# Optimization experiments

Hardware: AMD Instinct MI355X
Metric: run time of the kernel (lower is better)

The kernel has to match this reference:

```python
import jax, jax.numpy as jnp
import numpy as np

B, S, D, H, DFF = 2, 2048, 2048, 16, 8192
DH = D // H
EPS = 1e-5


def _layer_norm(x, g, b):
    mu = jnp.mean(x, axis=-1, keepdims=True)
    var = jnp.mean(jnp.square(x - mu), axis=-1, keepdims=True)
    return (x - mu) * jax.lax.rsqrt(var + EPS) * g + b


def setup_inputs() -> dict:
    key = jax.random.key(0)
    ks = jax.random.split(key, 12)
    sc = 0.02
    inp = {
        "x": jax.random.normal(ks[0], (B, S, D), dtype=jnp.float32),
        # attention projections, stored [in, out] (torch Linear weight transposed)
        "wq": jax.random.normal(ks[1], (D, D), dtype=jnp.float32) * sc,
        "bq": jnp.zeros((D,), jnp.float32),
        "wk": jax.random.normal(ks[2], (D, D), dtype=jnp.float32) * sc,
        "bk": jnp.zeros((D,), jnp.float32),
        "wv": jax.random.normal(ks[3], (D, D), dtype=jnp.float32) * sc,
        "bv": jnp.zeros((D,), jnp.float32),
        "wo": jax.random.normal(ks[4], (D, D), dtype=jnp.float32) * sc,
        "bo": jnp.zeros((D,), jnp.float32),
        "ln1_g": jnp.ones((D,), jnp.float32),
        "ln1_b": jnp.zeros((D,), jnp.float32),
        # feed-forward
        "w1": jax.random.normal(ks[5], (D, DFF), dtype=jnp.float32) * sc,
        "b1": jnp.zeros((DFF,), jnp.float32),
        "w2": jax.random.normal(ks[6], (DFF, D), dtype=jnp.float32) * sc,
        "b2": jnp.zeros((D,), jnp.float32),
        "ln2_g": jnp.ones((D,), jnp.float32),
        "ln2_b": jnp.zeros((D,), jnp.float32),
    }
    return inp


def reference(x, wq, bq, wk, bk, wv, bv, wo, bo, ln1_g, ln1_b,
              w1, b1, w2, b2, ln2_g, ln2_b):
    # ---- MultiHeadAttentionBlock: x + MHA(LN(x)) ----
    h = _layer_norm(x, ln1_g, ln1_b)                      # [B,S,D]
    q = (h @ wq + bq).reshape(B, S, H, DH).transpose(0, 2, 1, 3)  # [B,H,S,DH]
    k = (h @ wk + bk).reshape(B, S, H, DH).transpose(0, 2, 1, 3)
    v = (h @ wv + bv).reshape(B, S, H, DH).transpose(0, 2, 1, 3)

    # faithful to source: scale by sqrt(d_dim), NOT sqrt(head_dim)
    scores = jnp.einsum("bhqd,bhkd->bhqk", q, k) / np.sqrt(D).astype(np.float32)
    # faithful triu/transpose masking (softmax sees raw zeros, not -inf)
    t = jnp.triu(scores).swapaxes(-2, -1)                 # [B,H,S,S]
    s = jax.nn.softmax(t, axis=-2)
    r = jnp.triu(s).swapaxes(-2, -1)
    attn = jnp.einsum("bhqk,bhkd->bhqd", r, v)            # [B,H,S,DH]
    attn = attn.transpose(0, 2, 1, 3).reshape(B, S, D)
    x = x + attn @ wo + bo

    # ---- FeedForwardBlock: x + FF(LN(x)), dropout rate 0 ----
    h2 = _layer_norm(x, ln2_g, ln2_b)
    ff = jax.nn.relu(h2 @ w1 + b1) @ w2 + b2
    return x + ff
```

## Files before the change

### kernel.cpp

```cpp
#include <hip/hip_runtime.h>


typedef unsigned short ushort_t;
typedef unsigned int   uint32;
typedef __attribute__((ext_vector_type(8)))  short    short8;
typedef __attribute__((ext_vector_type(8)))  ushort_t ushort8;
typedef __attribute__((ext_vector_type(4)))  float    f32x4;

#define BDIM   2
#define SEQ    2048
#define DMODEL 2048
#define NHEAD  16
#define DHEAD  128
#define DFFN   8192
#define MROWS  (BDIM*SEQ)
#define LDQKV  6144

#define GPTR(p) (const __attribute__((address_space(1))) void*)((const void*)(p))
#define SPTR(p) (__attribute__((address_space(3))) void*)((void*)(p))

__device__ __forceinline__ float bf2f(ushort_t u) {
  union { uint32 i; float f; } c; c.i = ((uint32)u) << 16; return c.f;
}
__device__ __forceinline__ ushort_t f2bf(float f) {
  union { float f; uint32 i; } c; c.f = f;
  uint32 u = c.i;
  return (ushort_t)((u + 0x7fffu + ((u >> 16) & 1u)) >> 16);
}

__global__ __launch_bounds__(256) void prep_kern(
    const float* __restrict__ wq, const float* __restrict__ wk,
    const float* __restrict__ wv, const float* __restrict__ wo,
    const float* __restrict__ w1, const float* __restrict__ w2,
    const float* __restrict__ bq, const float* __restrict__ bk,
    const float* __restrict__ bv,
    ushort_t* __restrict__ WQKV, ushort_t* __restrict__ WOT,
    ushort_t* __restrict__ W1T, ushort_t* __restrict__ W2T,
    float* __restrict__ Bcat)
{
  const int bid = blockIdx.x;
  if (bid >= 49152) {
    for (int i = threadIdx.x; i < 6144; i += 256)
      Bcat[i] = (i < 2048) ? bq[i] : ((i < 4096) ? bk[i - 2048] : bv[i - 4096]);
    return;
  }
  const float* W; ushort_t* Wt; int K, N, local;
  if (bid < 12288) {
    const int which = bid >> 12; local = bid & 4095;
    W = (which == 0) ? wq : (which == 1) ? wk : wv;
    Wt = WQKV + (size_t)which * 2048 * 2048; K = 2048; N = 2048;
  } else if (bid < 16384) { W = wo; Wt = WOT; K = 2048; N = 2048; local = bid - 12288; }
  else if (bid < 32768)   { W = w1; Wt = W1T; K = 2048; N = 8192; local = bid - 16384; }
  else                    { W = w2; Wt = W2T; K = 8192; N = 2048; local = bid - 32768; }
  const int ntiles = N >> 5;
  const int nb = (local % ntiles) * 32, kb = (local / ntiles) * 32;

  __shared__ float tile[32][33];
  const int tx = threadIdx.x & 31, ty = threadIdx.x >> 5;
#pragma unroll
  for (int j = 0; j < 32; j += 8)
    tile[ty + j][tx] = W[(size_t)(kb + ty + j) * N + nb + tx];
  __syncthreads();
#pragma unroll
  for (int j = 0; j < 32; j += 8)
    Wt[(size_t)(nb + ty + j) * K + kb + tx] = f2bf(tile[tx][ty + j]);
}

__global__ __launch_bounds__(256) void ln_kern(
    const float* __restrict__ X, const float* __restrict__ G,
    const float* __restrict__ Bb, ushort_t* __restrict__ Out)
{
  const int row = blockIdx.x, tid = threadIdx.x;
  const float* xr = X + (size_t)row * DMODEL;
  float4 v0 = ((const float4*)xr)[tid * 2];
  float4 v1 = ((const float4*)xr)[tid * 2 + 1];
  float s  = v0.x + v0.y + v0.z + v0.w + v1.x + v1.y + v1.z + v1.w;
  float ss = v0.x*v0.x + v0.y*v0.y + v0.z*v0.z + v0.w*v0.w
           + v1.x*v1.x + v1.y*v1.y + v1.z*v1.z + v1.w*v1.w;
#pragma unroll
  for (int off = 32; off > 0; off >>= 1) {
    s  += __shfl_down(s, off);
    ss += __shfl_down(ss, off);
  }
  __shared__ float rs[4], rss[4];
  __shared__ float sh_mu, sh_rst;
  const int wv = tid >> 6;
  if ((tid & 63) == 0) { rs[wv] = s; rss[wv] = ss; }
  __syncthreads();
  if (tid == 0) {
    float S1 = rs[0] + rs[1] + rs[2] + rs[3];
    float S2 = rss[0] + rss[1] + rss[2] + rss[3];
    float mu = S1 * (1.f / DMODEL);
    float var = S2 * (1.f / DMODEL) - mu * mu;
    sh_mu = mu;
    sh_rst = rsqrtf(var + 1e-5f);
  }
  __syncthreads();
  const float mu = sh_mu, rst = sh_rst;
  float4 g0 = ((const float4*)G)[tid * 2];
  float4 g1 = ((const float4*)G)[tid * 2 + 1];
  float4 b0 = ((const float4*)Bb)[tid * 2];
  float4 b1 = ((const float4*)Bb)[tid * 2 + 1];
  ushort8 o;
  o[0] = f2bf((v0.x - mu) * rst * g0.x + b0.x);
  o[1] = f2bf((v0.y - mu) * rst * g0.y + b0.y);
  o[2] = f2bf((v0.z - mu) * rst * g0.z + b0.z);
  o[3] = f2bf((v0.w - mu) * rst * g0.w + b0.w);
  o[4] = f2bf((v1.x - mu) * rst * g1.x + b1.x);
  o[5] = f2bf((v1.y - mu) * rst * g1.y + b1.y);
  o[6] = f2bf((v1.z - mu) * rst * g1.z + b1.z);
  o[7] = f2bf((v1.w - mu) * rst * g1.w + b1.w);
  *(ushort8*)(Out + (size_t)row * DMODEL + tid * 8) = o;
}

__global__ __launch_bounds__(256) void combine_ln_kern(
    const ushort_t* __restrict__ pp, const float* __restrict__ bias,
    const float* __restrict__ xres, const float* __restrict__ G,
    const float* __restrict__ Bb, float* __restrict__ X2,
    ushort_t* __restrict__ Out)
{
  const int row = blockIdx.x, tid = threadIdx.x;
  const size_t i = (size_t)row * DMODEL + tid * 8;
  ushort8 p0 = *(const ushort8*)(pp + i);
  ushort8 p1 = *(const ushort8*)(pp + (size_t)MROWS * 2048 + i);
  float v[8];
#pragma unroll
  for (int j = 0; j < 8; ++j)
    v[j] = bf2f(p0[j]) + bf2f(p1[j]) + bias[tid * 8 + j] + xres[i + j];
  float4 o0 = {v[0], v[1], v[2], v[3]}, o1 = {v[4], v[5], v[6], v[7]};
  *(float4*)(X2 + i) = o0;
  *(float4*)(X2 + i + 4) = o1;

  float s = 0.f, ss = 0.f;
#pragma unroll
  for (int j = 0; j < 8; ++j) { s += v[j]; ss += v[j] * v[j]; }
#pragma unroll
  for (int off = 32; off > 0; off >>= 1) {
    s  += __shfl_down(s, off);
    ss += __shfl_down(ss, off);
  }
  __shared__ float rs[4], rss[4];
  __shared__ float sh_mu, sh_rst;
  const int wvv = tid >> 6;
  if ((tid & 63) == 0) { rs[wvv] = s; rss[wvv] = ss; }
  __syncthreads();
  if (tid == 0) {
    float S1 = rs[0] + rs[1] + rs[2] + rs[3];
    float S2 = rss[0] + rss[1] + rss[2] + rss[3];
    float mu = S1 * (1.f / DMODEL);
    float var = S2 * (1.f / DMODEL) - mu * mu;
    sh_mu = mu; sh_rst = rsqrtf(var + 1e-5f);
  }
  __syncthreads();
  const float mu = sh_mu, rst = sh_rst;
  ushort8 o;
#pragma unroll
  for (int j = 0; j < 8; ++j)
    o[j] = f2bf((v[j] - mu) * rst * G[tid * 8 + j] + Bb[tid * 8 + j]);
  *(ushort8*)(Out + i) = o;
}

template<int OUT, int RELU, int KDIV>
__global__ __launch_bounds__(512, 2) void gemm8_kern(
    const ushort_t* __restrict__ A, const ushort_t* __restrict__ Bt,
    const float* __restrict__ bias, void* __restrict__ Cout,
    int M, int N, int K)
{
  __shared__ ushort_t sA[4 * 8192];
  __shared__ ushort_t sB[4 * 8192];

  const int tid = threadIdx.x;
  const int nM  = gridDim.y;
  const int nwg = gridDim.x * nM;
  const int bid = blockIdx.y * gridDim.x + blockIdx.x;
  const int cpx = nwg >> 3;
  const int swz = (bid & 7) * cpx + (bid >> 3);
  const int m0 = (swz % nM) * 256;
  const int n0 = (swz / nM) * 256;

  const int Keff = K / KDIV;
  const int k0 = (KDIV > 1) ? blockIdx.z * Keff : 0;
  const int T = Keff >> 6;

  const int l = tid & 63, w = tid >> 6;
  const int lr = l & 15, lg = l >> 4;
  const int wr = w >> 2, wc = w & 3;

  const int xch   = (lg ^ ((lr >> 1) & 3)) * 8;
  const int abase = (wr * 128 + lr) * 32 + xch;
  const int bbase = (wc * 64  + lr) * 32 + xch;

  const int sr = tid >> 2;
  const int sg = ((tid & 3) ^ ((tid >> 3) & 3)) * 8;
  const ushort_t* Asrc = A  + (size_t)(m0 + sr) * K + k0 + sg;
  const ushort_t* Bsrc = Bt + (size_t)(n0 + sr) * K + k0 + sg;
  ushort_t* dA = sA + tid * 8;
  ushort_t* dB = sB + tid * 8;

#define SA_(slot, kt, kk, r) __builtin_amdgcn_global_load_lds( \
    GPTR(Asrc + (size_t)(r) * 128 * K + (kt) * 64 + (kk) * 32), \
    SPTR(dA + (slot) * 8192 + (r) * 4096), 16, 0, 0)
#define SB_(slot, kt, kk, r) __builtin_amdgcn_global_load_lds( \
    GPTR(Bsrc + (size_t)(r) * 128 * K + (kt) * 64 + (kk) * 32), \
    SPTR(dB + (slot) * 8192 + (r) * 4096), 16, 0, 0)

  f32x4 acc[8][4] = {};

  SA_(0, 0, 0, 0); SA_(0, 0, 0, 1); SB_(0, 0, 0, 0); SB_(0, 0, 0, 1);
  SA_(1, 0, 1, 0); SA_(1, 0, 1, 1); SB_(1, 0, 1, 0); SB_(1, 0, 1, 1);
  SA_(2, 1, 0, 0); SA_(2, 1, 0, 1); SB_(2, 1, 0, 0); SB_(2, 1, 0, 1);
  asm volatile("s_waitcnt vmcnt(8)" ::: "memory");
  __builtin_amdgcn_s_barrier();

  for (int t = 0; t < T; ++t) {
    const int c = t & 1;
    const ushort_t* A0 = sA + (c * 2 + 0) * 8192;
    const ushort_t* B0 = sB + (c * 2 + 0) * 8192;
    const ushort_t* A1 = sA + (c * 2 + 1) * 8192;
    const ushort_t* B1 = sB + (c * 2 + 1) * 8192;
    const int s1 = (c ^ 1) * 2 + 1;
    const int s0 = c * 2;
    const bool pf1 = (t + 1 < T), pf0 = (t + 2 < T);
    const bool last2 = (t >= T - 2);

    short8 a0, a1, a2, a3, b0, b1, b2, b3;

    b0 = *(const short8*)(B0 + bbase);
    b1 = *(const short8*)(B0 + bbase + 512);
    b2 = *(const short8*)(B0 + bbase + 1024);
    b3 = *(const short8*)(B0 + bbase + 1536);
    a0 = *(const short8*)(A0 + abase);
    a1 = *(const short8*)(A0 + abase + 512);
    a2 = *(const short8*)(A0 + abase + 1024);
    a3 = *(const short8*)(A0 + abase + 1536);
    if (pf1) { SA_(s1, t + 1, 1, 0); SA_(s1, t + 1, 1, 1); }
    __builtin_amdgcn_s_barrier();
    asm volatile("s_waitcnt lgkmcnt(0)" ::: "memory");
    __builtin_amdgcn_s_setprio(1);
    acc[0][0] = __builtin_amdgcn_mfma_f32_16x16x32_bf16(a0, b0, acc[0][0], 0, 0, 0);
    acc[0][1] = __builtin_amdgcn_mfma_f32_16x16x32_bf16(a0, b1, acc[0][1], 0, 0, 0);
    acc[0][2] = __builtin_amdgcn_mfma_f32_16x16x32_bf16(a0, b2, acc[0][2], 0, 0, 0);
    acc[0][3] = __builtin_amdgcn_mfma_f32_16x16x32_bf16(a0, b3, acc[0][3], 0, 0, 0);
    acc[1][0] = __builtin_amdgcn_mfma_f32_16x16x32_bf16(a1, b0, acc[1][0], 0, 0, 0);
    acc[1][1] = __builtin_amdgcn_mfma_f32_16x16x32_bf16(a1, b1, acc[1][1], 0, 0, 0);
    acc[1][2] = __builtin_amdgcn_mfma_f32_16x16x32_bf16(a1, b2, acc[1][2], 0, 0, 0);
    acc[1][3] = __builtin_amdgcn_mfma_f32_16x16x32_bf16(a1, b3, acc[1][3], 0, 0, 0);
    acc[2][0] = __builtin_amdgcn_mfma_f32_16x16x32_bf16(a2, b0, acc[2][0], 0, 0, 0);
    acc[2][1] = __builtin_amdgcn_mfma_f32_16x16x32_bf16(a2, b1, acc[2][1], 0, 0, 0);
    acc[2][2] = __builtin_amdgcn_mfma_f32_16x16x32_bf16(a2, b2, acc[2][2], 0, 0, 0);
    acc[2][3] = __builtin_amdgcn_mfma_f32_16x16x32_bf16(a2, b3, acc[2][3], 0, 0, 0);
    acc[3][0] = __builtin_amdgcn_mfma_f32_16x16x32_bf16(a3, b0, acc[3][0], 0, 0, 0);
    acc[3][1] = __builtin_amdgcn_mfma_f32_16x16x32_bf16(a3, b1, acc[3][1], 0, 0, 0);
    acc[3][2] = __builtin_amdgcn_mfma_f32_16x16x32_bf16(a3, b2, acc[3][2], 0, 0, 0);
    acc[3][3] = __builtin_amdgcn_mfma_f32_16x16x32_bf16(a3, b3, acc[3][3], 0, 0, 0);
    __builtin_amdgcn_s_setprio(0);
    __builtin_amdgcn_s_barrier();

    a0 = *(const short8*)(A0 + abase + 2048);
    a1 = *(const short8*)(A0 + abase + 2560);
    a2 = *(const short8*)(A0 + abase + 3072);
    a3 = *(const short8*)(A0 + abase + 3584);
    if (pf1) { SB_(s1, t + 1, 1, 0); SB_(s1, t + 1, 1, 1); }
    __builtin_amdgcn_s_barrier();
    asm volatile("s_waitcnt lgkmcnt(0)" ::: "memory");
    __builtin_amdgcn_s_setprio(1);
    acc[4][0] = __builtin_amdgcn_mfma_f32_16x16x32_bf16(a0, b0, acc[4][0], 0, 0, 0);
    acc[4][1] = __builtin_amdgcn_mfma_f32_16x16x32_bf16(a0, b1, acc[4][1], 0, 0, 0);
    acc[4][2] = __builtin_amdgcn_mfma_f32_16x16x32_bf16(a0, b2, acc[4][2], 0, 0, 0);
    acc[4][3] = __builtin_amdgcn_mfma_f32_16x16x32_bf16(a0, b3, acc[4][3], 0, 0, 0);
    acc[5][0] = __builtin_amdgcn_mfma_f32_16x16x32_bf16(a1, b0, acc[5][0], 0, 0, 0);
    acc[5][1] = __builtin_amdgcn_mfma_f32_16x16x32_bf16(a1, b1, acc[5][1], 0, 0, 0);
    acc[5][2] = __builtin_amdgcn_mfma_f32_16x16x32_bf16(a1, b2, acc[5][2], 0, 0, 0);
    acc[5][3] = __builtin_amdgcn_mfma_f32_16x16x32_bf16(a1, b3, acc[5][3], 0, 0, 0);
    acc[6][0] = __builtin_amdgcn_mfma_f32_16x16x32_bf16(a2, b0, acc[6][0], 0, 0, 0);
    acc[6][1] = __builtin_amdgcn_mfma_f32_16x16x32_bf16(a2, b1, acc[6][1], 0, 0, 0);
    acc[6][2] = __builtin_amdgcn_mfma_f32_16x16x32_bf16(a2, b2, acc[6][2], 0, 0, 0);
    acc[6][3] = __builtin_amdgcn_mfma_f32_16x16x32_bf16(a2, b3, acc[6][3], 0, 0, 0);
    acc[7][0] = __builtin_amdgcn_mfma_f32_16x16x32_bf16(a3, b0, acc[7][0], 0, 0, 0);
    acc[7][1] = __builtin_amdgcn_mfma_f32_16x16x32_bf16(a3, b1, acc[7][1], 0, 0, 0);
    acc[7][2] = __builtin_amdgcn_mfma_f32_16x16x32_bf16(a3, b2, acc[7][2], 0, 0, 0);
    acc[7][3] = __builtin_amdgcn_mfma_f32_16x16x32_bf16(a3, b3, acc[7][3], 0, 0, 0);
    __builtin_amdgcn_s_setprio(0);
    if (!last2) { asm volatile("s_waitcnt vmcnt(8)" ::: "memory"); }
    else        { asm volatile("s_waitcnt vmcnt(0)" ::: "memory"); }
    __builtin_amdgcn_s_barrier();

    b0 = *(const short8*)(B1 + bbase);
    b1 = *(const short8*)(B1 + bbase + 512);
    b2 = *(const short8*)(B1 + bbase + 1024);
    b3 = *(const short8*)(B1 + bbase + 1536);
    a0 = *(const short8*)(A1 + abase);
    a1 = *(const short8*)(A1 + abase + 512);
    a2 = *(const short8*)(A1 + abase + 1024);
    a3 = *(const short8*)(A1 + abase + 1536);
    if (pf0) { SA_(s0, t + 2, 0, 0); SA_(s0, t + 2, 0, 1); }
    __builtin_amdgcn_s_barrier();
    asm volatile("s_waitcnt lgkmcnt(0)" ::: "memory");
    __builtin_amdgcn_s_setprio(1);
    acc[0][0] = __builtin_amdgcn_mfma_f32_16x16x32_bf16(a0, b0, acc[0][0], 0, 0, 0);
    acc[0][1] = __builtin_amdgcn_mfma_f32_16x16x32_bf16(a0, b1, acc[0][1], 0, 0, 0);
    acc[0][2] = __builtin_amdgcn_mfma_f32_16x16x32_bf16(a0, b2, acc[0][2], 0, 0, 0);
    acc[0][3] = __builtin_amdgcn_mfma_f32_16x16x32_bf16(a0, b3, acc[0][3], 0, 0, 0);
    acc[1][0] = __builtin_amdgcn_mfma_f32_16x16x32_bf16(a1, b0, acc[1][0], 0, 0, 0);
    acc[1][1] = __builtin_amdgcn_mfma_f32_16x16x32_bf16(a1, b1, acc[1][1], 0, 0, 0);
    acc[1][2] = __builtin_amdgcn_mfma_f32_16x16x32_bf16(a1, b2, acc[1][2], 0, 0, 0);
    acc[1][3] = __builtin_amdgcn_mfma_f32_16x16x32_bf16(a1, b3, acc[1][3], 0, 0, 0);
    acc[2][0] = __builtin_amdgcn_mfma_f32_16x16x32_bf16(a2, b0, acc[2][0], 0, 0, 0);
    acc[2][1] = __builtin_amdgcn_mfma_f32_16x16x32_bf16(a2, b1, acc[2][1], 0, 0, 0);
    acc[2][2] = __builtin_amdgcn_mfma_f32_16x16x32_bf16(a2, b2, acc[2][2], 0, 0, 0);
    acc[2][3] = __builtin_amdgcn_mfma_f32_16x16x32_bf16(a2, b3, acc[2][3], 0, 0, 0);
    acc[3][0] = __builtin_amdgcn_mfma_f32_16x16x32_bf16(a3, b0, acc[3][0], 0, 0, 0);
    acc[3][1] = __builtin_amdgcn_mfma_f32_16x16x32_bf16(a3, b1, acc[3][1], 0, 0, 0);
    acc[3][2] = __builtin_amdgcn_mfma_f32_16x16x32_bf16(a3, b2, acc[3][2], 0, 0, 0);
    acc[3][3] = __builtin_amdgcn_mfma_f32_16x16x32_bf16(a3, b3, acc[3][3], 0, 0, 0);
    __builtin_amdgcn_s_setprio(0);
    __builtin_amdgcn_s_barrier();

    a0 = *(const short8*)(A1 + abase + 2048);
    a1 = *(const short8*)(A1 + abase + 2560);
    a2 = *(const short8*)(A1 + abase + 3072);
    a3 = *(const short8*)(A1 + abase + 3584);
    if (pf0) { SB_(s0, t + 2, 0, 0); SB_(s0, t + 2, 0, 1); }
    __builtin_amdgcn_s_barrier();
    asm volatile("s_waitcnt lgkmcnt(0)" ::: "memory");
    __builtin_amdgcn_s_setprio(1);
    acc[4][0] = __builtin_amdgcn_mfma_f32_16x16x32_bf16(a0, b0, acc[4][0], 0, 0, 0);
    acc[4][1] = __builtin_amdgcn_mfma_f32_16x16x32_bf16(a0, b1, acc[4][1], 0, 0, 0);
    acc[4][2] = __builtin_amdgcn_mfma_f32_16x16x32_bf16(a0, b2, acc[4][2], 0, 0, 0);
    acc[4][3] = __builtin_amdgcn_mfma_f32_16x16x32_bf16(a0, b3, acc[4][3], 0, 0, 0);
    acc[5][0] = __builtin_amdgcn_mfma_f32_16x16x32_bf16(a1, b0, acc[5][0], 0, 0, 0);
    acc[5][1] = __builtin_amdgcn_mfma_f32_16x16x32_bf16(a1, b1, acc[5][1], 0, 0, 0);
    acc[5][2] = __builtin_amdgcn_mfma_f32_16x16x32_bf16(a1, b2, acc[5][2], 0, 0, 0);
    acc[5][3] = __builtin_amdgcn_mfma_f32_16x16x32_bf16(a1, b3, acc[5][3], 0, 0, 0);
    acc[6][0] = __builtin_amdgcn_mfma_f32_16x16x32_bf16(a2, b0, acc[6][0], 0, 0, 0);
    acc[6][1] = __builtin_amdgcn_mfma_f32_16x16x32_bf16(a2, b1, acc[6][1], 0, 0, 0);
    acc[6][2] = __builtin_amdgcn_mfma_f32_16x16x32_bf16(a2, b2, acc[6][2], 0, 0, 0);
    acc[6][3] = __builtin_amdgcn_mfma_f32_16x16x32_bf16(a2, b3, acc[6][3], 0, 0, 0);
    acc[7][0] = __builtin_amdgcn_mfma_f32_16x16x32_bf16(a3, b0, acc[7][0], 0, 0, 0);
    acc[7][1] = __builtin_amdgcn_mfma_f32_16x16x32_bf16(a3, b1, acc[7][1], 0, 0, 0);
    acc[7][2] = __builtin_amdgcn_mfma_f32_16x16x32_bf16(a3, b2, acc[7][2], 0, 0, 0);
    acc[7][3] = __builtin_amdgcn_mfma_f32_16x16x32_bf16(a3, b3, acc[7][3], 0, 0, 0);
    __builtin_amdgcn_s_setprio(0);
    if (!last2) { asm volatile("s_waitcnt vmcnt(8)" ::: "memory"); }
    else        { asm volatile("s_waitcnt vmcnt(0)" ::: "memory"); }
    __builtin_amdgcn_s_barrier();
  }
#undef SA_
#undef SB_

  ushort_t* Pz = (OUT == 2)
      ? (ushort_t*)Cout + (size_t)blockIdx.z * M * N : (ushort_t*)Cout;
#pragma unroll
  for (int mi = 0; mi < 8; ++mi) {
#pragma unroll
    for (int ni = 0; ni < 4; ++ni) {
      const int gn = n0 + wc * 64 + ni * 16 + lr;
      const float bvv = (OUT == 2) ? 0.f : bias[gn];
#pragma unroll
      for (int j = 0; j < 4; ++j) {
        const int gm = m0 + wr * 128 + mi * 16 + lg * 4 + j;
        float v = acc[mi][ni][j] + bvv;
        if (RELU) v = fmaxf(v, 0.f);
        Pz[(size_t)gm * N + gn] = f2bf(v);
      }
    }
  }
}

__global__ __launch_bounds__(256) void combine_kern(
    const ushort_t* __restrict__ pp, const float* __restrict__ bias,
    const float* __restrict__ resid, float* __restrict__ out)
{
  const size_t i = ((size_t)blockIdx.x * 256 + threadIdx.x) * 8;
  ushort8 p0 = *(const ushort8*)(pp + i);
  ushort8 p1 = *(const ushort8*)(pp + (size_t)MROWS * 2048 + i);
  const int col = (int)(i & 2047);
  float4 r0 = *(const float4*)(resid + i);
  float4 r1 = *(const float4*)(resid + i + 4);
  float4 c0 = *(const float4*)(bias + col);
  float4 c1 = *(const float4*)(bias + col + 4);
  float4 o0, o1;
  o0.x = bf2f(p0[0]) + bf2f(p1[0]) + c0.x + r0.x;
  o0.y = bf2f(p0[1]) + bf2f(p1[1]) + c0.y + r0.y;
  o0.z = bf2f(p0[2]) + bf2f(p1[2]) + c0.z + r0.z;
  o0.w = bf2f(p0[3]) + bf2f(p1[3]) + c0.w + r0.w;
  o1.x = bf2f(p0[4]) + bf2f(p1[4]) + c1.x + r1.x;
  o1.y = bf2f(p0[5]) + bf2f(p1[5]) + c1.y + r1.y;
  o1.z = bf2f(p0[6]) + bf2f(p1[6]) + c1.z + r1.z;
  o1.w = bf2f(p0[7]) + bf2f(p1[7]) + c1.w + r1.w;
  *(float4*)(out + i) = o0;
  *(float4*)(out + i + 4) = o1;
}

__global__ __launch_bounds__(256) void attn_stats_kern(
    const ushort_t* __restrict__ Q, const ushort_t* __restrict__ Kb,
    float* __restrict__ E, float* __restrict__ DG, int ld)
{
  __shared__ ushort_t Ksm[64 * 128];
  const int qb = blockIdx.x;
  const int bh = blockIdx.y;
  const int b = bh >> 4, h = bh & 15;
  const int tid = threadIdx.x;
  const int l = tid & 63, w = tid >> 6;
  const int lr = l & 15, lg = l >> 4;

  const int qrow0 = qb * 128 + w * 32;

  short8 af[2][4];
#pragma unroll
  for (int g = 0; g < 2; ++g) {
    const size_t qoff = (size_t)(b * SEQ + qrow0 + g * 16 + lr) * ld + h * DHEAD + lg * 8;
#pragma unroll
    for (int c = 0; c < 4; ++c) af[g][c] = *(const short8*)(Q + qoff + c * 32);
  }

  const int srow_b = w * 16 + (l >> 4);
  const ushort_t* Kg = Kb + (size_t)b * SEQ * ld + (size_t)h * DHEAD;
  ushort_t* Sbase = Ksm + w * 2048;

  f32x4 sume[2] = {{0.f,0.f,0.f,0.f},{0.f,0.f,0.f,0.f}};
  f32x4 dge[2]  = {{0.f,0.f,0.f,0.f},{0.f,0.f,0.f,0.f}};
  const float scale = 0.0220970869120796f;
  const int rx = lr & 7;

  for (int kc = qb * 2; kc < 32; ++kc) {
    __syncthreads();
#pragma unroll
    for (int c = 0; c < 4; ++c) {
      const int row = srow_b + c * 4;
      const int g = (l & 15) ^ (row & 7);
      __builtin_amdgcn_global_load_lds(
          GPTR(Kg + (size_t)(kc * 64 + row) * ld + g * 8),
          SPTR(Sbase + c * 512), 16, 0, 0);
    }
    __syncthreads();

    for (int ks = 0; ks < 4; ++ks) {
      const int kbase = kc * 64 + ks * 16;
      if (kbase + 16 <= qrow0) continue;
      short8 bfr[4];
#pragma unroll
      for (int c = 0; c < 4; ++c)
        bfr[c] = *(const short8*)(Ksm + (ks * 16 + lr) * 128 + ((lg + c * 4) ^ rx) * 8);
#pragma unroll
      for (int g = 0; g < 2; ++g) {
        const int qg = qrow0 + g * 16;
        if (kbase < qg) continue;
        f32x4 sc = {0.f, 0.f, 0.f, 0.f};
        sc = __builtin_amdgcn_mfma_f32_16x16x32_bf16(af[g][0], bfr[0], sc, 0, 0, 0);
        sc = __builtin_amdgcn_mfma_f32_16x16x32_bf16(af[g][1], bfr[1], sc, 0, 0, 0);
        sc = __builtin_amdgcn_mfma_f32_16x16x32_bf16(af[g][2], bfr[2], sc, 0, 0, 0);
        sc = __builtin_amdgcn_mfma_f32_16x16x32_bf16(af[g][3], bfr[3], sc, 0, 0, 0);
        if (kbase == qg) {
          const int ki = kbase + lr;
#pragma unroll
          for (int j = 0; j < 4; ++j) {
            const int qi = qg + lg * 4 + j;
            if (ki >= qi) {
              float e = __expf(sc[j] * scale);
              sume[g][j] += e;
              if (ki == qi) dge[g][j] += e;
            }
          }
        } else {
#pragma unroll
          for (int j = 0; j < 4; ++j)
            sume[g][j] += __expf(sc[j] * scale);
        }
      }
    }
  }

#pragma unroll
  for (int g = 0; g < 2; ++g) {
#pragma unroll
    for (int j = 0; j < 4; ++j) {
#pragma unroll
      for (int off = 1; off < 16; off <<= 1) {
        sume[g][j] += __shfl_xor(sume[g][j], off);
        dge[g][j]  += __shfl_xor(dge[g][j], off);
      }
    }
  }
  if (lr == 0) {
#pragma unroll
    for (int g = 0; g < 2; ++g)
#pragma unroll
      for (int j = 0; j < 4; ++j) {
        E[(size_t)bh * SEQ + qrow0 + g * 16 + lg * 4 + j]  = sume[g][j];
        DG[(size_t)bh * SEQ + qrow0 + g * 16 + lg * 4 + j] = dge[g][j];
      }
  }
}

__global__ __launch_bounds__(128) void vchunk_kern(
    const ushort_t* __restrict__ V, float* __restrict__ CS, int ld)
{
  const int c = blockIdx.x, bh = blockIdx.y;
  const int b = bh >> 4, h = bh & 15;
  const int dh = threadIdx.x;
  const ushort_t* vp = V + (size_t)(b * SEQ + c * 64) * ld + h * DHEAD + dh;
  float s = 0.f;
  for (int i = 0; i < 64; ++i) s += bf2f(vp[(size_t)i * ld]);
  CS[((size_t)bh * 32 + c) * 128 + dh] = s;
}

__global__ __launch_bounds__(128) void attn_combine_kern(
    const ushort_t* __restrict__ V, const float* __restrict__ CS,
    const float* __restrict__ E, const float* __restrict__ DG,
    ushort_t* __restrict__ Attn, int ldv)
{
  const int c = blockIdx.x, bh = blockIdx.y;
  const int b = bh >> 4, h = bh & 15;
  const int dh = threadIdx.x;
  float prefix = 0.f;
  for (int cc = 0; cc < c; ++cc) prefix += CS[((size_t)bh * 32 + cc) * 128 + dh];
  const ushort_t* vp = V + (size_t)(b * SEQ + c * 64) * ldv + h * DHEAD + dh;
  ushort_t* ap = Attn + (size_t)(b * SEQ + c * 64) * DMODEL + h * DHEAD + dh;
  const int qb = c * 64;
  for (int i = 0; i < 64; ++i) {
    const int qq = qb + i;
    const float denom = (float)qq + E[(size_t)bh * SEQ + qq];
    const float de = DG[(size_t)bh * SEQ + qq];
    const float vv = bf2f(vp[(size_t)i * ldv]);
    ap[(size_t)i * DMODEL] = f2bf((prefix + de * vv) / denom);
    prefix += vv;
  }
}

extern "C" void kernel_launch(void* const* d_in, const int* in_sizes, int n_in,
                              void* d_out, int out_size, void* d_ws, size_t ws_size,
                              hipStream_t stream)
{
  const float* x    = (const float*)d_in[0];
  const float* wq   = (const float*)d_in[1];
  const float* bq   = (const float*)d_in[2];
  const float* wk   = (const float*)d_in[3];
  const float* bk   = (const float*)d_in[4];
  const float* wv   = (const float*)d_in[5];
  const float* bv   = (const float*)d_in[6];
  const float* wo   = (const float*)d_in[7];
  const float* bo   = (const float*)d_in[8];
  const float* ln1g = (const float*)d_in[9];
  const float* ln1b = (const float*)d_in[10];
  const float* w1   = (const float*)d_in[11];
  const float* b1   = (const float*)d_in[12];
  const float* w2   = (const float*)d_in[13];
  const float* b2   = (const float*)d_in[14];
  const float* ln2g = (const float*)d_in[15];
  const float* ln2b = (const float*)d_in[16];
  float* out = (float*)d_out;

  char* ws = (char*)d_ws;
  ushort_t* W1T  = (ushort_t*)(ws + 0);
  ushort_t* PPf2 = (ushort_t*)(ws + 0);
  ushort_t* W2T  = (ushort_t*)(ws + 33554432);
  ushort_t* WOT  = (ushort_t*)(ws + 67108864);
  float*    X2   = (float*)   (ws + 75497472);
  float*    Bcat = (float*)   (ws + 75497472);
  ushort_t* Hb   = (ushort_t*)(ws + 109051904);
  ushort_t* F1   = (ushort_t*)(ws + 125829120);
  ushort_t* PPwo = (ushort_t*)(ws + 125829120);
  ushort_t* WQKV = (ushort_t*)(ws + 125829120);
  ushort_t* QKVb = (ushort_t*)(ws + 150994944);
  float*    Eb   = (float*)   (ws + 201326592);
  float*    DGb  = (float*)   (ws + 201588736);
  float*    CSb  = (float*)   (ws + 201850880);

  prep_kern<<<49153, 256, 0, stream>>>(wq, wk, wv, wo, w1, w2, bq, bk, bv,
                                       WQKV, WOT, W1T, W2T, Bcat);

  ln_kern<<<MROWS, 256, 0, stream>>>(x, ln1g, ln1b, Hb);

  gemm8_kern<1, 0, 1><<<dim3(24, 16), 512, 0, stream>>>(
      Hb, WQKV, Bcat, QKVb, MROWS, LDQKV, DMODEL);

  attn_stats_kern<<<dim3(16, 32), 256, 0, stream>>>(QKVb, QKVb + 2048, Eb, DGb, LDQKV);

  vchunk_kern<<<dim3(32, 32), 128, 0, stream>>>(QKVb + 4096, CSb, LDQKV);
  attn_combine_kern<<<dim3(32, 32), 128, 0, stream>>>(QKVb + 4096, CSb, Eb, DGb, Hb, LDQKV);

  gemm8_kern<2, 0, 2><<<dim3(8, 16, 2), 512, 0, stream>>>(
      Hb, WOT, bo, PPwo, MROWS, DMODEL, DMODEL);

  combine_ln_kern<<<MROWS, 256, 0, stream>>>(PPwo, bo, x, ln2g, ln2b, X2, Hb);

  gemm8_kern<1, 1, 1><<<dim3(32, 16), 512, 0, stream>>>(
      Hb, W1T, b1, F1, MROWS, DFFN, DMODEL);

  gemm8_kern<2, 0, 2><<<dim3(8, 16, 2), 512, 0, stream>>>(
      F1, W2T, b2, PPf2, MROWS, DMODEL, DFFN);
  combine_kern<<<4096, 256, 0, stream>>>(PPf2, b2, X2, out);
}
```

Before: 661.0 us.

## Drop intra-stage barriers in gemm8 and add triple-buffered 128x256 GEMM for FFN1

Removes the extra s_barrier and lgkmcnt waits around each MFMA half-step in the main GEMM kernel. Waves can then overlap their LDS reads and prefetch issue instead of lock-stepping. Adds a new GEMM kernel used only for the FFN up-projection, with a 128x256 tile, a 3-slot LDS ring buffer, a single barrier per K-step, and twice as many workgroups. The barrier removal relies on the remaining barriers still guarding slot reuse, so a hidden LDS race is a risk.

```diff
diff --git a/kernel.cpp b/kernel.cpp
--- a/kernel.cpp
+++ b/kernel.cpp
@@ -234,8 +234,6 @@
     a2 = *(const short8*)(A0 + abase + 1024);
     a3 = *(const short8*)(A0 + abase + 1536);
     if (pf1) { SA_(s1, t + 1, 1, 0); SA_(s1, t + 1, 1, 1); }
-    __builtin_amdgcn_s_barrier();
-    asm volatile("s_waitcnt lgkmcnt(0)" ::: "memory");
     __builtin_amdgcn_s_setprio(1);
     acc[0][0] = __builtin_amdgcn_mfma_f32_16x16x32_bf16(a0, b0, acc[0][0], 0, 0, 0);
     acc[0][1] = __builtin_amdgcn_mfma_f32_16x16x32_bf16(a0, b1, acc[0][1], 0, 0, 0);
@@ -254,15 +252,12 @@
     acc[3][2] = __builtin_amdgcn_mfma_f32_16x16x32_bf16(a3, b2, acc[3][2], 0, 0, 0);
     acc[3][3] = __builtin_amdgcn_mfma_f32_16x16x32_bf16(a3, b3, acc[3][3], 0, 0, 0);
     __builtin_amdgcn_s_setprio(0);
-    __builtin_amdgcn_s_barrier();
 
     a0 = *(const short8*)(A0 + abase + 2048);
     a1 = *(const short8*)(A0 + abase + 2560);
     a2 = *(const short8*)(A0 + abase + 3072);
     a3 = *(const short8*)(A0 + abase + 3584);
     if (pf1) { SB_(s1, t + 1, 1, 0); SB_(s1, t + 1, 1, 1); }
-    __builtin_amdgcn_s_barrier();
-    asm volatile("s_waitcnt lgkmcnt(0)" ::: "memory");
     __builtin_amdgcn_s_setprio(1);
     acc[4][0] = __builtin_amdgcn_mfma_f32_16x16x32_bf16(a0, b0, acc[4][0], 0, 0, 0);
     acc[4][1] = __builtin_amdgcn_mfma_f32_16x16x32_bf16(a0, b1, acc[4][1], 0, 0, 0);
@@ -294,8 +289,6 @@
     a2 = *(const short8*)(A1 + abase + 1024);
     a3 = *(const short8*)(A1 + abase + 1536);
     if (pf0) { SA_(s0, t + 2, 0, 0); SA_(s0, t + 2, 0, 1); }
-    __builtin_amdgcn_s_barrier();
-    asm volatile("s_waitcnt lgkmcnt(0)" ::: "memory");
     __builtin_amdgcn_s_setprio(1);
     acc[0][0] = __builtin_amdgcn_mfma_f32_16x16x32_bf16(a0, b0, acc[0][0], 0, 0, 0);
     acc[0][1] = __builtin_amdgcn_mfma_f32_16x16x32_bf16(a0, b1, acc[0][1], 0, 0, 0);
@@ -314,15 +307,12 @@
     acc[3][2] = __builtin_amdgcn_mfma_f32_16x16x32_bf16(a3, b2, acc[3][2], 0, 0, 0);
     acc[3][3] = __builtin_amdgcn_mfma_f32_16x16x32_bf16(a3, b3, acc[3][3], 0, 0, 0);
     __builtin_amdgcn_s_setprio(0);
-    __builtin_amdgcn_s_barrier();
 
     a0 = *(const short8*)(A1 + abase + 2048);
     a1 = *(const short8*)(A1 + abase + 2560);
     a2 = *(const short8*)(A1 + abase + 3072);
     a3 = *(const short8*)(A1 + abase + 3584);
     if (pf0) { SB_(s0, t + 2, 0, 0); SB_(s0, t + 2, 0, 1); }
-    __builtin_amdgcn_s_barrier();
-    asm volatile("s_waitcnt lgkmcnt(0)" ::: "memory");
     __builtin_amdgcn_s_setprio(1);
     acc[4][0] = __builtin_amdgcn_mfma_f32_16x16x32_bf16(a0, b0, acc[4][0], 0, 0, 0);
     acc[4][1] = __builtin_amdgcn_mfma_f32_16x16x32_bf16(a0, b1, acc[4][1], 0, 0, 0);
@@ -367,6 +357,98 @@
   }
 }
 
+template<int RELU>
+__global__ __launch_bounds__(512) void gemm_hi_kern(
+    const ushort_t* __restrict__ A, const ushort_t* __restrict__ Bt,
+    const float* __restrict__ bias, ushort_t* __restrict__ Cout,
+    int M, int N, int K)
+{
+  __shared__ ushort_t sA[3 * 4096];
+  __shared__ ushort_t sB[3 * 8192];
+
+  const int tid = threadIdx.x;
+  const int nM  = gridDim.y;
+  const int nwg = gridDim.x * nM;
+  const int bid = blockIdx.y * gridDim.x + blockIdx.x;
+  const int cpx = nwg >> 3;
+  const int swz = (bid & 7) * cpx + (bid >> 3);
+  const int m0 = (swz % nM) * 128;
+  const int n0 = (swz / nM) * 256;
+
+  const int l = tid & 63, w = tid >> 6;
+  const int lr = l & 15, lg = l >> 4;
+  const int wr = w >> 2, wc = w & 3;
+
+  const int xch   = (lg ^ ((lr >> 1) & 3)) * 8;
+  const int abase = (wr * 64 + lr) * 32 + xch;
+  const int bbase = (wc * 64 + lr) * 32 + xch;
+
+  const int sr = tid >> 2;
+  const int sg = ((tid & 3) ^ ((tid >> 3) & 3)) * 8;
+  const ushort_t* Asrc = A  + (size_t)(m0 + sr) * K + sg;
+  const ushort_t* Bsrc = Bt + (size_t)(n0 + sr) * K + sg;
+  ushort_t* dA = sA + tid * 8;
+  ushort_t* dB = sB + tid * 8;
+
+  const int U = K >> 5;
+
+#define SAU(slot, u) __builtin_amdgcn_global_load_lds( \
+    GPTR(Asrc + (size_t)(u) * 32), SPTR(dA + (slot) * 4096), 16, 0, 0)
+#define SBU(slot, u, r) __builtin_amdgcn_global_load_lds( \
+    GPTR(Bsrc + (size_t)(r) * 128 * K + (size_t)(u) * 32), \
+    SPTR(dB + (slot) * 8192 + (r) * 4096), 16, 0, 0)
+
+  f32x4 acc[4][4] = {};
+
+  SAU(0, 0); SBU(0, 0, 0); SBU(0, 0, 1);
+  SAU(1, 1); SBU(1, 1, 0); SBU(1, 1, 1);
+  asm volatile("s_waitcnt vmcnt(3)" ::: "memory");
+  __builtin_amdgcn_s_barrier();
+
+  int cur = 0;
+  for (int u = 0; u < U; ++u) {
+    const ushort_t* pA = sA + cur * 4096;
+    const ushort_t* pB = sB + cur * 8192;
+    const int nx = (cur == 0) ? 2 : cur - 1;
+    short8 af[4], bf[4];
+#pragma unroll
+    for (int i = 0; i < 4; ++i) af[i] = *(const short8*)(pA + abase + i * 512);
+#pragma unroll
+    for (int i = 0; i < 4; ++i) bf[i] = *(const short8*)(pB + bbase + i * 512);
+    if (u + 2 < U) { SAU(nx, u + 2); SBU(nx, u + 2, 0); SBU(nx, u + 2, 1); }
+    __builtin_amdgcn_s_setprio(1);
+#pragma unroll
+    for (int mi = 0; mi < 4; ++mi)
+#pragma unroll
+      for (int ni = 0; ni < 4; ++ni)
+        acc[mi][ni] = __builtin_amdgcn_mfma_f32_16x16x32_bf16(
+            af[mi], bf[ni], acc[mi][ni], 0, 0, 0);
+    __builtin_amdgcn_s_setprio(0);
+    if (u < U - 2) { asm volatile("s_waitcnt vmcnt(3)" ::: "memory"); }
+    else           { asm volatile("s_waitcnt vmcnt(0)" ::: "memory"); }
+    __builtin_amdgcn_s_barrier();
+    cur = (cur == 2) ? 0 : cur + 1;
+  }
+#undef SAU
+#undef SBU
+
+#pragma unroll
+  for (int mi = 0; mi < 4; ++mi) {
+#pragma unroll
+    for (int ni = 0; ni < 4; ++ni) {
+      const int gn = n0 + wc * 64 + ni * 16 + lr;
+      const float bvv = bias[gn];
+#pragma unroll
+      for (int j = 0; j < 4; ++j) {
+        const int gm = m0 + wr * 64 + mi * 16 + lg * 4 + j;
+        float v = acc[mi][ni][j] + bvv;
+        if (RELU) v = fmaxf(v, 0.f);
+        Cout[(size_t)gm * N + gn] = f2bf(v);
+      }
+    }
+  }
+}
+
 __global__ __launch_bounds__(256) void combine_kern(
     const ushort_t* __restrict__ pp, const float* __restrict__ bias,
     const float* __restrict__ resid, float* __restrict__ out)
@@ -585,7 +667,7 @@
 
   combine_ln_kern<<<MROWS, 256, 0, stream>>>(PPwo, bo, x, ln2g, ln2b, X2, Hb);
 
-  gemm8_kern<1, 1, 1><<<dim3(32, 16), 512, 0, stream>>>(
+  gemm_hi_kern<1><<<dim3(32, 32), 512, 0, stream>>>(
       Hb, W1T, b1, F1, MROWS, DFFN, DMODEL);
 
   gemm8_kern<2, 0, 2><<<dim3(8, 16, 2), 512, 0, stream>>>(
```

New measurement: 631.4 us. -4.5%, faster.
